# Performance work log

Hardware: AMD Instinct MI355X
Metric: run time of the kernel (lower is better)

## Reference

```python
import jax, jax.numpy as jnp
import numpy as np

S, B, D, E = 257, 64, 768, 8
H = 4 * D  # expert hidden dim

def quick_gelu(x):
    return x * jax.nn.sigmoid(1.702 * x)

def setup_inputs() -> dict:
    key = jax.random.key(0)
    ks = jax.random.split(key, 7)
    scale = 1.0 / np.sqrt(D)
    return {
        "x": jax.random.normal(ks[0], (S, B, D), dtype=jnp.float32),
        "W1": jax.random.normal(ks[1], (E, H, D), dtype=jnp.float32) * scale,   # fc1 weight per expert (out,in)
        "b1": jax.random.normal(ks[2], (E, H), dtype=jnp.float32) * 0.01,
        "W2": jax.random.normal(ks[3], (E, D, H), dtype=jnp.float32) * (1.0 / np.sqrt(H)),
        "b2": jax.random.normal(ks[4], (E, D), dtype=jnp.float32) * 0.01,
        "Wr": jax.random.normal(ks[5], (E, D), dtype=jnp.float32) * scale,       # router weight (E, d)
        "br": jnp.zeros((E,), dtype=jnp.float32),
    }

def reference(x, W1, b1, W2, b2, Wr, br):
    s, b, d = x.shape
    xf = x.reshape(s * b, d)                                  # [T, d]
    logits = xf @ Wr.T + br                                   # [T, E]
    probs = jax.nn.softmax(logits, axis=-1)                   # [T, E]
    # all-experts MLP, batched over the expert axis
    h = jnp.einsum('td,ehd->teh', xf, W1) + b1                # [T, E, 4d]
    h = quick_gelu(h)
    outs = jnp.einsum('teh,edh->ted', h, W2) + b2             # [T, E, d]
    y = jnp.einsum('ted,te->td', outs, probs)                 # router-weighted combine
    return y.reshape(s, b, d)
```

## Files before the change

kernel.cpp:

```cpp
#include <hip/hip_runtime.h>

typedef unsigned short u16;
typedef float f32x4 __attribute__((ext_vector_type(4)));
typedef short s16x8 __attribute__((ext_vector_type(8)));

#define T_TOK   16448L
#define D_DIM   768L
#define H_DIM   3072L
#define E_NUM   8L
#define M_PAD   16640L

__device__ __forceinline__ u16 f2bf(float f){
  unsigned u = __float_as_uint(f);
  u = u + 0x7FFFu + ((u >> 16) & 1u);
  return (u16)(u >> 16);
}
__device__ __forceinline__ unsigned f2bf2(float a, float b){
  return (unsigned)f2bf(a) | ((unsigned)f2bf(b) << 16);
}

__device__ __forceinline__ void gload_lds16(const u16* g, u16* s){
  __builtin_amdgcn_global_load_lds((const __attribute__((address_space(1))) void*)g,
                                   (__attribute__((address_space(3))) void*)s,
                                   16, 0, 0);
}

__device__ __forceinline__ int xcd_chunk(int idx, int n){
  const int q = n >> 3, r = n & 7, x = idx & 7;
  return (x < r ? x*(q+1) : r*(q+1) + (x-r)*q) + (idx >> 3);
}

__global__ void k_conv(const float* __restrict__ in, u16* __restrict__ outp,
                       long nValid, long nTotal){
  long i = (long)blockIdx.x * blockDim.x + threadIdx.x;
  long stride = (long)gridDim.x * blockDim.x;
  long n8 = nTotal >> 3;
  for (long v = i; v < n8; v += stride){
    long base = v << 3;
    uint4 o;
    if (base < nValid){
      const float4 f0 = *(const float4*)(in + base);
      const float4 f1 = *(const float4*)(in + base + 4);
      o.x = f2bf2(f0.x, f0.y); o.y = f2bf2(f0.z, f0.w);
      o.z = f2bf2(f1.x, f1.y); o.w = f2bf2(f1.z, f1.w);
    } else {
      o.x = 0u; o.y = 0u; o.z = 0u; o.w = 0u;
    }
    *(uint4*)(outp + base) = o;
  }
}

__global__ void k_router(const float* __restrict__ x, const float* __restrict__ Wr,
                         const float* __restrict__ br, float* __restrict__ probs){
  int w = (int)((blockIdx.x * (long)blockDim.x + threadIdx.x) >> 6);
  int lane = threadIdx.x & 63;
  if (w >= (int)T_TOK) return;
  const float* xr = x + (long)w * D_DIM;
  float l[8];
#pragma unroll
  for (int e = 0; e < 8; ++e) l[e] = 0.f;
#pragma unroll
  for (int c = 0; c < 3; ++c){
    const float4 xv = *(const float4*)(xr + c*256 + lane*4);
#pragma unroll
    for (int e = 0; e < 8; ++e){
      const float4 wv = *(const float4*)(Wr + (long)e*D_DIM + c*256 + lane*4);
      l[e] += xv.x*wv.x + xv.y*wv.y + xv.z*wv.z + xv.w*wv.w;
    }
  }
#pragma unroll
  for (int e = 0; e < 8; ++e){
#pragma unroll
    for (int off = 32; off > 0; off >>= 1) l[e] += __shfl_xor(l[e], off);
    l[e] += br[e];
  }
  float m = l[0];
#pragma unroll
  for (int e = 1; e < 8; ++e) m = fmaxf(m, l[e]);
  float s = 0.f;
#pragma unroll
  for (int e = 0; e < 8; ++e){ l[e] = __expf(l[e] - m); s += l[e]; }
  float inv = 1.f / s;
  if (lane == 0){
    float4 p0 = { l[0]*inv, l[1]*inv, l[2]*inv, l[3]*inv };
    float4 p1 = { l[4]*inv, l[5]*inv, l[6]*inv, l[7]*inv };
    *(float4*)(probs + (long)w*8)     = p0;
    *(float4*)(probs + (long)w*8 + 4) = p1;
  }
}

__device__ __forceinline__ void stage256(const u16* __restrict__ gbase, long ldk,
                                         u16* sbase, int l, int w){
  const int rw = l >> 3;
  const int c8 = (l & 7) ^ rw;
  const u16* g = gbase + (long)(w*8 + rw) * ldk + c8*8;
  u16* s = sbase + w*512;
#pragma unroll
  for (int i = 0; i < 4; ++i)
    gload_lds16(g + (long)(i*64) * ldk, s + i*4096);
}

__device__ __forceinline__ s16x8 ld_frag(const u16* S, int rbase, int c, int ln){
  const int r = rbase + ln;
  return *(const s16x8*)(S + (r << 6) + ((c ^ (r & 7)) << 3));
}

#define FENCE()  __builtin_amdgcn_sched_barrier(0)
#define BAR()    do{ FENCE(); __builtin_amdgcn_s_barrier(); FENCE(); }while(0)

__device__ __forceinline__ void gemm256(const u16* __restrict__ Ag, long lda,
                                        const u16* __restrict__ Bg, long ldb,
                                        int NT, u16* lds0, u16* lds1,
                                        int tid, f32x4 (&acc)[8][4]){
  const int l  = tid & 63, w = tid >> 6;
  const int wr = w >> 2,  wc = w & 3;
  const int g4 = l >> 4,  ln = l & 15;
  u16* cur = lds0; u16* nxt = lds1;

  stage256(Ag,       lda, cur,         l, w);
  stage256(Bg,       ldb, cur + 16384, l, w);
  stage256(Ag + 64,  lda, nxt,         l, w);
  stage256(Bg + 64,  ldb, nxt + 16384, l, w);
  FENCE();
  asm volatile("s_waitcnt vmcnt(8)" ::: "memory");
  BAR();

  for (int kt = 0; kt < NT; ++kt){
    const u16* As = cur;
    const u16* Bs = cur + 16384;
    s16x8 a0[8], b0[4], a1[8], b1[4];

#pragma unroll
    for (int ni = 0; ni < 4; ++ni) b0[ni] = ld_frag(Bs, wc*64 + ni*16, g4, ln);
#pragma unroll
    for (int mi = 0; mi < 8; ++mi) a0[mi] = ld_frag(As, wr*128 + mi*16, g4, ln);
#pragma unroll
    for (int mi = 0; mi < 8; ++mi)
#pragma unroll
      for (int ni = 0; ni < 4; ++ni)
        acc[mi][ni] = __builtin_amdgcn_mfma_f32_16x16x32_bf16(a0[mi], b0[ni], acc[mi][ni], 0, 0, 0);
#pragma unroll
    for (int ni = 0; ni < 4; ++ni) b1[ni] = ld_frag(Bs, wc*64 + ni*16, 4 + g4, ln);
#pragma unroll
    for (int mi = 0; mi < 8; ++mi) a1[mi] = ld_frag(As, wr*128 + mi*16, 4 + g4, ln);
#pragma unroll
    for (int mi = 0; mi < 8; ++mi)
#pragma unroll
      for (int ni = 0; ni < 4; ++ni)
        acc[mi][ni] = __builtin_amdgcn_mfma_f32_16x16x32_bf16(a1[mi], b1[ni], acc[mi][ni], 0, 0, 0);

    BAR();
    if (kt + 2 < NT){
      stage256(Ag + (long)(kt+2)*64, lda, cur,         l, w);
      stage256(Bg + (long)(kt+2)*64, ldb, cur + 16384, l, w);
      FENCE();
      asm volatile("s_waitcnt vmcnt(8)" ::: "memory");
    } else {
      FENCE();
      asm volatile("s_waitcnt vmcnt(0)" ::: "memory");
    }
    BAR();
    u16* t = cur; cur = nxt; nxt = t;
  }
}

__global__ __launch_bounds__(512, 2) void k_pair(const u16* __restrict__ xb,
                                                 const u16* __restrict__ w1b,
                                                 const float* __restrict__ b1,
                                                 const u16* __restrict__ w2b,
                                                 const float* __restrict__ b2,
                                                 const float* __restrict__ probs,
                                                 float* __restrict__ out,
                                                 const u16* __restrict__ hbR,
                                                 u16* __restrict__ hbW,
                                                 int e2, int t02,
                                                 int e1, int t01, int mt1, int n2){
  __shared__ alignas(16) u16 lds[2][32768];
  const int tid = threadIdx.x;
  const int l  = tid & 63, w = tid >> 6;
  const int wr = w >> 2,  wc = w & 3;
  const int g4 = l >> 4,  ln = l & 15;
  const int bx = (int)blockIdx.x;
  f32x4 acc[8][4] = {};

  if (bx < n2){
    const int wg = xcd_chunk(bx, n2);
    const int tx = wg / 3, ty = wg % 3;
    const int m0 = tx << 8, n0 = ty << 8;
    gemm256(hbR + (long)m0 * H_DIM, H_DIM,
            w2b + ((long)e2 * D_DIM + n0) * H_DIM, H_DIM,
            48, &lds[0][0], &lds[1][0], tid, acc);
    float bias[4];
#pragma unroll
    for (int ni = 0; ni < 4; ++ni) bias[ni] = b2[(long)e2*D_DIM + n0 + wc*64 + ni*16 + ln];
#pragma unroll
    for (int mi = 0; mi < 8; ++mi){
#pragma unroll
      for (int j = 0; j < 4; ++j){
        const int gt = t02 + m0 + wr*128 + mi*16 + g4*4 + j;
        if (gt < (int)T_TOK){
          const float p = probs[(long)gt*8 + e2];
          float* dst = out + (long)gt * D_DIM + n0 + wc*64;
#pragma unroll
          for (int ni = 0; ni < 4; ++ni){
            const float v = p * (acc[mi][ni][j] + bias[ni]);
            if (e2 == 0) dst[ni*16 + ln] = v;
            else         dst[ni*16 + ln] += v;
          }
        }
      }
    }
  } else {
    const int n1 = (int)gridDim.x - n2;
    const int wg = xcd_chunk(bx - n2, n1);
    const int tx = wg % mt1, ty = wg / mt1;
    const int m0 = tx << 8, n0 = ty << 8;
    gemm256(xb + (long)(t01 + m0) * D_DIM, D_DIM,
            w1b + ((long)e1 * H_DIM + n0) * D_DIM, D_DIM,
            12, &lds[0][0], &lds[1][0], tid, acc);
    float bias[4];
#pragma unroll
    for (int ni = 0; ni < 4; ++ni) bias[ni] = b1[(long)e1*H_DIM + n0 + wc*64 + ni*16 + ln];
#pragma unroll
    for (int mi = 0; mi < 8; ++mi){
#pragma unroll
      for (int j = 0; j < 4; ++j){
        const int r = m0 + wr*128 + mi*16 + g4*4 + j;
        u16* dst = hbW + (long)r * H_DIM + n0 + wc*64;
#pragma unroll
        for (int ni = 0; ni < 4; ++ni){
          const float v  = acc[mi][ni][j] + bias[ni];
          const float gl = v / (1.0f + __expf(-1.702f * v));
          dst[ni*16 + ln] = f2bf(gl);
        }
      }
    }
  }
}

extern "C" void kernel_launch(void* const* d_in, const int* in_sizes, int n_in,
                              void* d_out, int out_size, void* d_ws, size_t ws_size,
                              hipStream_t stream){
  const float* x  = (const float*)d_in[0];
  const float* W1 = (const float*)d_in[1];
  const float* b1 = (const float*)d_in[2];
  const float* W2 = (const float*)d_in[3];
  const float* b2 = (const float*)d_in[4];
  const float* Wr = (const float*)d_in[5];
  const float* br = (const float*)d_in[6];
  float* out = (float*)d_out;

  char* ws = (char*)d_ws;
  size_t off = 0;
  auto carve = [&](size_t bytes)->void*{
    void* p = ws + off; off += (bytes + 255) & ~(size_t)255; return p;
  };
  u16*   xb    = (u16*)  carve((size_t)M_PAD * D_DIM * 2);
  u16*   w1b   = (u16*)  carve((size_t)E_NUM * H_DIM * D_DIM * 2);
  u16*   w2b   = (u16*)  carve((size_t)E_NUM * D_DIM * H_DIM * 2);
  float* probs = (float*)carve((size_t)T_TOK * E_NUM * 4);
  u16*   hbA   = (u16*)  carve((size_t)8192 * H_DIM * 2);
  u16*   hbB   = (u16*)  carve((size_t)8448 * H_DIM * 2);

  k_conv<<<dim3(2048), dim3(256), 0, stream>>>(x,  xb,  T_TOK*D_DIM, M_PAD*D_DIM);
  k_conv<<<dim3(2048), dim3(256), 0, stream>>>(W1, w1b, E_NUM*H_DIM*D_DIM, E_NUM*H_DIM*D_DIM);
  k_conv<<<dim3(2048), dim3(256), 0, stream>>>(W2, w2b, E_NUM*D_DIM*H_DIM, E_NUM*D_DIM*H_DIM);
  k_router<<<dim3(4112), dim3(256), 0, stream>>>(x, Wr, br, probs);

  const int MTA = 32, MTB = 33;
  const int T0A = 0,  T0B = 8192;

  auto pair = [&](int e2, const u16* hbR, int t02, int mt2,
                  int e1, u16* hbW, int t01, int mt1){
    const int n2 = mt2 * 3, n1 = mt1 * 12;
    k_pair<<<dim3((unsigned)(n2 + n1)), dim3(512), 0, stream>>>(
        xb, w1b, b1, w2b, b2, probs, out, hbR, hbW,
        e2, t02, e1, t01, mt1, n2);
  };

  pair(0, nullptr, 0, 0, 0, hbA, T0A, MTA);
  for (int e = 0; e < 8; ++e){
    pair(e, hbA, T0A, MTA, e, hbB, T0B, MTB);
    if (e < 7) pair(e, hbB, T0B, MTB, e + 1, hbA, T0A, MTA);
  }
  pair(7, hbB, T0B, MTB, 0, nullptr, 0, 0);
}
```

Before: 2.104 ms.

## Switch GEMM mainloop to K=32 tiles with a four-stage LDS ring

Replaces the double-buffered K=64 staging in the shared 256x256 GEMM with K=32 slices held in a four-deep LDS ring buffer, using a new XOR swizzle and precomputed fragment offsets. Loads are issued three stages ahead with vmcnt waits that taper off near the tail. The goal is to hide more global-load latency behind the MFMAs. The cost is twice as many loop iterations and barriers, and less MFMA work per barrier.

```diff
diff --git a/kernel.cpp b/kernel.cpp
--- a/kernel.cpp
+++ b/kernel.cpp
@@ -89,78 +89,79 @@
   }
 }
 
-__device__ __forceinline__ void stage256(const u16* __restrict__ gbase, long ldk,
-                                         u16* sbase, int l, int w){
-  const int rw = l >> 3;
-  const int c8 = (l & 7) ^ rw;
-  const u16* g = gbase + (long)(w*8 + rw) * ldk + c8*8;
-  u16* s = sbase + w*512;
-#pragma unroll
-  for (int i = 0; i < 4; ++i)
-    gload_lds16(g + (long)(i*64) * ldk, s + i*4096);
-}
-
-__device__ __forceinline__ s16x8 ld_frag(const u16* S, int rbase, int c, int ln){
-  const int r = rbase + ln;
-  return *(const s16x8*)(S + (r << 6) + ((c ^ (r & 7)) << 3));
-}
-
 #define FENCE()  __builtin_amdgcn_sched_barrier(0)
 #define BAR()    do{ FENCE(); __builtin_amdgcn_s_barrier(); FENCE(); }while(0)
 
-__device__ __forceinline__ void gemm256(const u16* __restrict__ Ag, long lda,
-                                        const u16* __restrict__ Bg, long ldb,
-                                        int NT, u16* lds0, u16* lds1,
-                                        int tid, f32x4 (&acc)[8][4]){
+__device__ __forceinline__ void gemm256_k32(const u16* __restrict__ Ag, long lda,
+                                            const u16* __restrict__ Bg, long ldb,
+                                            int NT, u16* lds, int tid,
+                                            f32x4 (&acc)[8][4]){
   const int l  = tid & 63, w = tid >> 6;
   const int wr = w >> 2,  wc = w & 3;
   const int g4 = l >> 4,  ln = l & 15;
-  u16* cur = lds0; u16* nxt = lds1;
-
-  stage256(Ag,       lda, cur,         l, w);
-  stage256(Bg,       ldb, cur + 16384, l, w);
-  stage256(Ag + 64,  lda, nxt,         l, w);
-  stage256(Bg + 64,  ldb, nxt + 16384, l, w);
+
+  const int rw16 = l >> 2;
+  const int scol = ((l & 3) ^ (rw16 & 3)) << 3;
+  const u16* gA0 = Ag + (long)(      w*16 + rw16) * lda + scol;
+  const u16* gA1 = Ag + (long)(128 + w*16 + rw16) * lda + scol;
+  const u16* gB0 = Bg + (long)(      w*16 + rw16) * ldb + scol;
+  const u16* gB1 = Bg + (long)(128 + w*16 + rw16) * ldb + scol;
+  u16* dA0 = lds +        w*512;
+  u16* dA1 = lds + 4096 + w*512;
+  u16* dB0 = lds + 8192 +        w*512;
+  u16* dB1 = lds + 8192 + 4096 + w*512;
+
+  const int sw = (g4 ^ (ln & 3)) << 3;
+  int offA[8], offB[4];
+#pragma unroll
+  for (int mi = 0; mi < 8; ++mi) offA[mi] = (wr*128 + mi*16 + ln)*32 + sw;
+#pragma unroll
+  for (int ni = 0; ni < 4; ++ni) offB[ni] = 8192 + (wc*64 + ni*16 + ln)*32 + sw;
+
+#pragma unroll
+  for (int t = 0; t < 4; ++t){
+    const long ko = (long)t * 32;
+    const int  bo = t * 16384;
+    gload_lds16(gA0 + ko, dA0 + bo);
+    gload_lds16(gA1 + ko, dA1 + bo);
+    gload_lds16(gB0 + ko, dB0 + bo);
+    gload_lds16(gB1 + ko, dB1 + bo);
+  }
   FENCE();
-  asm volatile("s_waitcnt vmcnt(8)" ::: "memory");
+  asm volatile("s_waitcnt vmcnt(12)" ::: "memory");
   BAR();
 
   for (int kt = 0; kt < NT; ++kt){
-    const u16* As = cur;
-    const u16* Bs = cur + 16384;
-    s16x8 a0[8], b0[4], a1[8], b1[4];
-
-#pragma unroll
-    for (int ni = 0; ni < 4; ++ni) b0[ni] = ld_frag(Bs, wc*64 + ni*16, g4, ln);
-#pragma unroll
-    for (int mi = 0; mi < 8; ++mi) a0[mi] = ld_frag(As, wr*128 + mi*16, g4, ln);
+    const u16* base = lds + (kt & 3) * 16384;
+    s16x8 a[8], b[4];
+#pragma unroll
+    for (int ni = 0; ni < 4; ++ni) b[ni] = *(const s16x8*)(base + offB[ni]);
+#pragma unroll
+    for (int mi = 0; mi < 8; ++mi) a[mi] = *(const s16x8*)(base + offA[mi]);
 #pragma unroll
     for (int mi = 0; mi < 8; ++mi)
 #pragma unroll
       for (int ni = 0; ni < 4; ++ni)
-        acc[mi][ni] = __builtin_amdgcn_mfma_f32_16x16x32_bf16(a0[mi], b0[ni], acc[mi][ni], 0, 0, 0);
-#pragma unroll
-    for (int ni = 0; ni < 4; ++ni) b1[ni] = ld_frag(Bs, wc*64 + ni*16, 4 + g4, ln);
-#pragma unroll
-    for (int mi = 0; mi < 8; ++mi) a1[mi] = ld_frag(As, wr*128 + mi*16, 4 + g4, ln);
-#pragma unroll
-    for (int mi = 0; mi < 8; ++mi)
-#pragma unroll
-      for (int ni = 0; ni < 4; ++ni)
-        acc[mi][ni] = __builtin_amdgcn_mfma_f32_16x16x32_bf16(a1[mi], b1[ni], acc[mi][ni], 0, 0, 0);
-
-    BAR();
-    if (kt + 2 < NT){
-      stage256(Ag + (long)(kt+2)*64, lda, cur,         l, w);
-      stage256(Bg + (long)(kt+2)*64, ldb, cur + 16384, l, w);
+        acc[mi][ni] = __builtin_amdgcn_mfma_f32_16x16x32_bf16(a[mi], b[ni], acc[mi][ni], 0, 0, 0);
+
+    if (kt + 1 < NT){
+      BAR();
+      if (kt + 4 < NT){
+        const long ko = (long)(kt + 4) * 32;
+        const int  bo = (kt & 3) * 16384;
+        gload_lds16(gA0 + ko, dA0 + bo);
+        gload_lds16(gA1 + ko, dA1 + bo);
+        gload_lds16(gB0 + ko, dB0 + bo);
+        gload_lds16(gB1 + ko, dB1 + bo);
+      }
       FENCE();
-      asm volatile("s_waitcnt vmcnt(8)" ::: "memory");
-    } else {
-      FENCE();
-      asm volatile("s_waitcnt vmcnt(0)" ::: "memory");
-    }
-    BAR();
-    u16* t = cur; cur = nxt; nxt = t;
+      const int rem = NT - kt - 2;
+      if      (rem >= 3) asm volatile("s_waitcnt vmcnt(12)" ::: "memory");
+      else if (rem == 2) asm volatile("s_waitcnt vmcnt(8)"  ::: "memory");
+      else if (rem == 1) asm volatile("s_waitcnt vmcnt(4)"  ::: "memory");
+      else               asm volatile("s_waitcnt vmcnt(0)"  ::: "memory");
+      BAR();
+    }
   }
 }
 
@@ -175,7 +176,7 @@
                                                  u16* __restrict__ hbW,
                                                  int e2, int t02,
                                                  int e1, int t01, int mt1, int n2){
-  __shared__ alignas(16) u16 lds[2][32768];
+  __shared__ alignas(16) u16 lds[65536];
   const int tid = threadIdx.x;
   const int l  = tid & 63, w = tid >> 6;
   const int wr = w >> 2,  wc = w & 3;
@@ -187,9 +188,9 @@
     const int wg = xcd_chunk(bx, n2);
     const int tx = wg / 3, ty = wg % 3;
     const int m0 = tx << 8, n0 = ty << 8;
-    gemm256(hbR + (long)m0 * H_DIM, H_DIM,
-            w2b + ((long)e2 * D_DIM + n0) * H_DIM, H_DIM,
-            48, &lds[0][0], &lds[1][0], tid, acc);
+    gemm256_k32(hbR + (long)m0 * H_DIM, H_DIM,
+                w2b + ((long)e2 * D_DIM + n0) * H_DIM, H_DIM,
+                96, lds, tid, acc);
     float bias[4];
 #pragma unroll
     for (int ni = 0; ni < 4; ++ni) bias[ni] = b2[(long)e2*D_DIM + n0 + wc*64 + ni*16 + ln];
@@ -215,9 +216,9 @@
     const int wg = xcd_chunk(bx - n2, n1);
     const int tx = wg % mt1, ty = wg / mt1;
     const int m0 = tx << 8, n0 = ty << 8;
-    gemm256(xb + (long)(t01 + m0) * D_DIM, D_DIM,
-            w1b + ((long)e1 * H_DIM + n0) * D_DIM, D_DIM,
-            12, &lds[0][0], &lds[1][0], tid, acc);
+    gemm256_k32(xb + (long)(t01 + m0) * D_DIM, D_DIM,
+                w1b + ((long)e1 * H_DIM + n0) * D_DIM, D_DIM,
+                24, lds, tid, acc);
     float bias[4];
 #pragma unroll
     for (int ni = 0; ni < 4; ++ni) bias[ni] = b1[(long)e1*H_DIM + n0 + wc*64 + ni*16 + ln];
```

Result: slower. 2.218 ms (+5.4%).

## Interleave global-to-LDS staging with four MFMA sub-phases per K tile

Applied to the files above, without the earlier changes.

Restructures the 256x256 GEMM main loop into four quarter phases, each loading a subset of A/B fragments, issuing a slice of the next tiles' global-to-LDS copies, then running 16 MFMAs under raised wave priority. The goal is to spread memory traffic across the compute and cut register pressure, since only 4 A fragments are live at a time instead of 8. In exchange it adds more barriers per K step and a more intricate vmcnt accounting, which could stall waves or race on LDS reuse if the counts are off.

```diff
diff --git a/kernel.cpp b/kernel.cpp
--- a/kernel.cpp
+++ b/kernel.cpp
@@ -89,79 +89,111 @@
   }
 }
 
-__device__ __forceinline__ void stage256(const u16* __restrict__ gbase, long ldk,
-                                         u16* sbase, int l, int w){
-  const int rw = l >> 3;
-  const int c8 = (l & 7) ^ rw;
-  const u16* g = gbase + (long)(w*8 + rw) * ldk + c8*8;
-  u16* s = sbase + w*512;
-#pragma unroll
-  for (int i = 0; i < 4; ++i)
-    gload_lds16(g + (long)(i*64) * ldk, s + i*4096);
-}
+#define FENCE()  __builtin_amdgcn_sched_barrier(0)
+#define BAR()    do{ FENCE(); __builtin_amdgcn_s_barrier(); FENCE(); }while(0)
+#define LGK0()   do{ asm volatile("s_waitcnt lgkmcnt(0)" ::: "memory"); FENCE(); }while(0)
 
 __device__ __forceinline__ s16x8 ld_frag(const u16* S, int rbase, int c, int ln){
   const int r = rbase + ln;
   return *(const s16x8*)(S + (r << 6) + ((c ^ (r & 7)) << 3));
 }
 
-#define FENCE()  __builtin_amdgcn_sched_barrier(0)
-#define BAR()    do{ FENCE(); __builtin_amdgcn_s_barrier(); FENCE(); }while(0)
-
 __device__ __forceinline__ void gemm256(const u16* __restrict__ Ag, long lda,
                                         const u16* __restrict__ Bg, long ldb,
-                                        int NT, u16* lds0, u16* lds1,
-                                        int tid, f32x4 (&acc)[8][4]){
+                                        int NT, u16* lds, int tid,
+                                        f32x4 (&acc)[8][4]){
   const int l  = tid & 63, w = tid >> 6;
   const int wr = w >> 2,  wc = w & 3;
   const int g4 = l >> 4,  ln = l & 15;
-  u16* cur = lds0; u16* nxt = lds1;
-
-  stage256(Ag,       lda, cur,         l, w);
-  stage256(Bg,       ldb, cur + 16384, l, w);
-  stage256(Ag + 64,  lda, nxt,         l, w);
-  stage256(Bg + 64,  ldb, nxt + 16384, l, w);
+
+  const int rw = l >> 3;
+  const int c8 = (l & 7) ^ rw;
+  const u16* gA = Ag + (long)(w*8 + rw) * lda + c8*8;
+  const u16* gB = Bg + (long)(w*8 + rw) * ldb + c8*8;
+  u16* s0 = lds + w*512;
+#define SA(par,T,rnd) gload_lds16(gA + (long)(T)*64 + (long)(rnd)*64*lda, s0 + (par)*32768 + (rnd)*4096)
+#define SB(par,T,rnd) gload_lds16(gB + (long)(T)*64 + (long)(rnd)*64*ldb, s0 + (par)*32768 + 16384 + (rnd)*4096)
+
+#pragma unroll
+  for (int i = 0; i < 4; ++i) SA(0,0,i);
+#pragma unroll
+  for (int i = 0; i < 4; ++i) SB(0,0,i);
+  SA(1,1,0); SB(1,1,0); SA(1,1,2); SB(1,1,1);
   FENCE();
-  asm volatile("s_waitcnt vmcnt(8)" ::: "memory");
+  asm volatile("s_waitcnt vmcnt(4)" ::: "memory");
   BAR();
 
   for (int kt = 0; kt < NT; ++kt){
-    const u16* As = cur;
-    const u16* Bs = cur + 16384;
-    s16x8 a0[8], b0[4], a1[8], b1[4];
+    const int par = kt & 1, oth = par ^ 1;
+    const u16* As = lds + par * 32768;
+    const u16* Bs = As + 16384;
+    const bool st1 = (kt + 1 < NT), st2 = (kt + 2 < NT);
+    s16x8 aL[4], aH[4], b0[4], b1[4];
 
 #pragma unroll
     for (int ni = 0; ni < 4; ++ni) b0[ni] = ld_frag(Bs, wc*64 + ni*16, g4, ln);
 #pragma unroll
-    for (int mi = 0; mi < 8; ++mi) a0[mi] = ld_frag(As, wr*128 + mi*16, g4, ln);
-#pragma unroll
-    for (int mi = 0; mi < 8; ++mi)
+    for (int mi = 0; mi < 4; ++mi) aL[mi] = ld_frag(As, wr*128 + mi*16, g4, ln);
+    if (st1){ SA(oth, kt+1, 1); SB(oth, kt+1, 2); }
+    BAR(); LGK0();
+    __builtin_amdgcn_s_setprio(1);
+#pragma unroll
+    for (int mi = 0; mi < 4; ++mi)
 #pragma unroll
       for (int ni = 0; ni < 4; ++ni)
-        acc[mi][ni] = __builtin_amdgcn_mfma_f32_16x16x32_bf16(a0[mi], b0[ni], acc[mi][ni], 0, 0, 0);
+        acc[mi][ni] = __builtin_amdgcn_mfma_f32_16x16x32_bf16(aL[mi], b0[ni], acc[mi][ni], 0, 0, 0);
+    __builtin_amdgcn_s_setprio(0);
+    BAR();
+
 #pragma unroll
     for (int ni = 0; ni < 4; ++ni) b1[ni] = ld_frag(Bs, wc*64 + ni*16, 4 + g4, ln);
 #pragma unroll
-    for (int mi = 0; mi < 8; ++mi) a1[mi] = ld_frag(As, wr*128 + mi*16, 4 + g4, ln);
-#pragma unroll
-    for (int mi = 0; mi < 8; ++mi)
+    for (int mi = 0; mi < 4; ++mi) aL[mi] = ld_frag(As, wr*128 + mi*16, 4 + g4, ln);
+    if (st1){ SA(oth, kt+1, 3); SB(oth, kt+1, 3); }
+    BAR(); LGK0();
+    __builtin_amdgcn_s_setprio(1);
+#pragma unroll
+    for (int mi = 0; mi < 4; ++mi)
 #pragma unroll
       for (int ni = 0; ni < 4; ++ni)
-        acc[mi][ni] = __builtin_amdgcn_mfma_f32_16x16x32_bf16(a1[mi], b1[ni], acc[mi][ni], 0, 0, 0);
-
+        acc[mi][ni] = __builtin_amdgcn_mfma_f32_16x16x32_bf16(aL[mi], b1[ni], acc[mi][ni], 0, 0, 0);
+    __builtin_amdgcn_s_setprio(0);
     BAR();
-    if (kt + 2 < NT){
-      stage256(Ag + (long)(kt+2)*64, lda, cur,         l, w);
-      stage256(Bg + (long)(kt+2)*64, ldb, cur + 16384, l, w);
+
+#pragma unroll
+    for (int mi = 0; mi < 4; ++mi) aH[mi] = ld_frag(As, wr*128 + 64 + mi*16, g4, ln);
+    if (st2){ SA(par, kt+2, 0); SB(par, kt+2, 0); }
+    BAR(); LGK0();
+    __builtin_amdgcn_s_setprio(1);
+#pragma unroll
+    for (int mi = 0; mi < 4; ++mi)
+#pragma unroll
+      for (int ni = 0; ni < 4; ++ni)
+        acc[mi+4][ni] = __builtin_amdgcn_mfma_f32_16x16x32_bf16(aH[mi], b0[ni], acc[mi+4][ni], 0, 0, 0);
+    __builtin_amdgcn_s_setprio(0);
+    BAR();
+
+#pragma unroll
+    for (int mi = 0; mi < 4; ++mi) aH[mi] = ld_frag(As, wr*128 + 64 + mi*16, 4 + g4, ln);
+    if (st2){ SA(par, kt+2, 2); SB(par, kt+2, 1); }
+    BAR(); LGK0();
+    __builtin_amdgcn_s_setprio(1);
+#pragma unroll
+    for (int mi = 0; mi < 4; ++mi)
+#pragma unroll
+      for (int ni = 0; ni < 4; ++ni)
+        acc[mi+4][ni] = __builtin_amdgcn_mfma_f32_16x16x32_bf16(aH[mi], b1[ni], acc[mi+4][ni], 0, 0, 0);
+    __builtin_amdgcn_s_setprio(0);
+
+    if (st1){
       FENCE();
-      asm volatile("s_waitcnt vmcnt(8)" ::: "memory");
-    } else {
-      FENCE();
-      asm volatile("s_waitcnt vmcnt(0)" ::: "memory");
-    }
-    BAR();
-    u16* t = cur; cur = nxt; nxt = t;
-  }
+      if (st2) asm volatile("s_waitcnt vmcnt(4)" ::: "memory");
+      else     asm volatile("s_waitcnt vmcnt(0)" ::: "memory");
+      BAR();
+    }
+  }
+#undef SA
+#undef SB
 }
 
 __global__ __launch_bounds__(512, 2) void k_pair(const u16* __restrict__ xb,
@@ -175,7 +207,7 @@
                                                  u16* __restrict__ hbW,
                                                  int e2, int t02,
                                                  int e1, int t01, int mt1, int n2){
-  __shared__ alignas(16) u16 lds[2][32768];
+  __shared__ alignas(16) u16 lds[65536];
   const int tid = threadIdx.x;
   const int l  = tid & 63, w = tid >> 6;
   const int wr = w >> 2,  wc = w & 3;
@@ -189,7 +221,7 @@
     const int m0 = tx << 8, n0 = ty << 8;
     gemm256(hbR + (long)m0 * H_DIM, H_DIM,
             w2b + ((long)e2 * D_DIM + n0) * H_DIM, H_DIM,
-            48, &lds[0][0], &lds[1][0], tid, acc);
+            48, lds, tid, acc);
     float bias[4];
 #pragma unroll
     for (int ni = 0; ni < 4; ++ni) bias[ni] = b2[(long)e2*D_DIM + n0 + wc*64 + ni*16 + ln];
@@ -217,7 +249,7 @@
     const int m0 = tx << 8, n0 = ty << 8;
     gemm256(xb + (long)(t01 + m0) * D_DIM, D_DIM,
             w1b + ((long)e1 * H_DIM + n0) * D_DIM, D_DIM,
-            12, &lds[0][0], &lds[1][0], tid, acc);
+            12, lds, tid, acc);
     float bias[4];
 #pragma unroll
     for (int ni = 0; ni < 4; ++ni) bias[ni] = b1[(long)e1*H_DIM + n0 + wc*64 + ni*16 + ln];
```

Result: faster. 2.003 ms (-4.8%).

## Shrink GEMM tiles to 128x128 with single-buffered LDS and 256-thread blocks

Applied to the files above, without the earlier changes.

Replaces the 256x256 double-buffered GEMM tile (512 threads, 128KB LDS, prefetch two stages ahead) with a 128x128 single-buffered tile using 4 waves and 32KB LDS, with precomputed swizzled fragment offsets. Grid sizes, token padding and hidden buffer sizes are adjusted to match the smaller tiles. This raises block count and occupancy and cuts per-block LDS and register use. In exchange it loses global-to-LDS prefetch overlap, since loads are now waited on with a barrier every k-step, and it lowers operand reuse per tile.

```diff
diff --git a/kernel.cpp b/kernel.cpp
--- a/kernel.cpp
+++ b/kernel.cpp
@@ -8,7 +8,7 @@
 #define D_DIM   768L
 #define H_DIM   3072L
 #define E_NUM   8L
-#define M_PAD   16640L
+#define M_PAD   16512L
 
 __device__ __forceinline__ u16 f2bf(float f){
   unsigned u = __float_as_uint(f);
@@ -89,115 +89,102 @@
   }
 }
 
-__device__ __forceinline__ void stage256(const u16* __restrict__ gbase, long ldk,
-                                         u16* sbase, int l, int w){
+__device__ __forceinline__ void gemm128(const u16* __restrict__ Ag, long lda,
+                                        const u16* __restrict__ Bg, long ldb,
+                                        int NT, u16* As, u16* Bs,
+                                        int tid, f32x4 (&acc)[4][4]){
+  const int l  = tid & 63, w = tid >> 6;
+  const int wr = w >> 1,  wc = w & 1;
+  const int g4 = l >> 4,  ln = l & 15;
+
   const int rw = l >> 3;
   const int c8 = (l & 7) ^ rw;
-  const u16* g = gbase + (long)(w*8 + rw) * ldk + c8*8;
-  u16* s = sbase + w*512;
-#pragma unroll
-  for (int i = 0; i < 4; ++i)
-    gload_lds16(g + (long)(i*64) * ldk, s + i*4096);
-}
-
-__device__ __forceinline__ s16x8 ld_frag(const u16* S, int rbase, int c, int ln){
-  const int r = rbase + ln;
-  return *(const s16x8*)(S + (r << 6) + ((c ^ (r & 7)) << 3));
-}
-
-#define FENCE()  __builtin_amdgcn_sched_barrier(0)
-#define BAR()    do{ FENCE(); __builtin_amdgcn_s_barrier(); FENCE(); }while(0)
-
-__device__ __forceinline__ void gemm256(const u16* __restrict__ Ag, long lda,
-                                        const u16* __restrict__ Bg, long ldb,
-                                        int NT, u16* lds0, u16* lds1,
-                                        int tid, f32x4 (&acc)[8][4]){
-  const int l  = tid & 63, w = tid >> 6;
-  const int wr = w >> 2,  wc = w & 3;
-  const int g4 = l >> 4,  ln = l & 15;
-  u16* cur = lds0; u16* nxt = lds1;
-
-  stage256(Ag,       lda, cur,         l, w);
-  stage256(Bg,       ldb, cur + 16384, l, w);
-  stage256(Ag + 64,  lda, nxt,         l, w);
-  stage256(Bg + 64,  ldb, nxt + 16384, l, w);
-  FENCE();
-  asm volatile("s_waitcnt vmcnt(8)" ::: "memory");
-  BAR();
+  const u16* pA = Ag + (long)(w*8 + rw) * lda + c8*8;
+  const u16* pB = Bg + (long)(w*8 + rw) * ldb + c8*8;
+  const long sA = 32 * lda, sB = 32 * ldb;
+  u16* dA = As + w*512;
+  u16* dB = Bs + w*512;
+
+  int offA[2][4], offB[2][4];
+#pragma unroll
+  for (int kk = 0; kk < 2; ++kk)
+#pragma unroll
+    for (int i = 0; i < 4; ++i){
+      const int co = (((kk<<2) | g4) ^ (ln & 7)) << 3;
+      offA[kk][i] = (wr*64 + i*16 + ln)*64 + co;
+      offB[kk][i] = (wc*64 + i*16 + ln)*64 + co;
+    }
 
   for (int kt = 0; kt < NT; ++kt){
-    const u16* As = cur;
-    const u16* Bs = cur + 16384;
-    s16x8 a0[8], b0[4], a1[8], b1[4];
-
-#pragma unroll
-    for (int ni = 0; ni < 4; ++ni) b0[ni] = ld_frag(Bs, wc*64 + ni*16, g4, ln);
-#pragma unroll
-    for (int mi = 0; mi < 8; ++mi) a0[mi] = ld_frag(As, wr*128 + mi*16, g4, ln);
-#pragma unroll
-    for (int mi = 0; mi < 8; ++mi)
+    gload_lds16(pA,        dA);
+    gload_lds16(pA +   sA, dA + 2048);
+    gload_lds16(pA + 2*sA, dA + 4096);
+    gload_lds16(pA + 3*sA, dA + 6144);
+    gload_lds16(pB,        dB);
+    gload_lds16(pB +   sB, dB + 2048);
+    gload_lds16(pB + 2*sB, dB + 4096);
+    gload_lds16(pB + 3*sB, dB + 6144);
+    pA += 64; pB += 64;
+    __syncthreads();
+
+    s16x8 a0[4], b0[4], a1[4], b1[4];
+#pragma unroll
+    for (int i = 0; i < 4; ++i) a0[i] = *(const s16x8*)(As + offA[0][i]);
+#pragma unroll
+    for (int i = 0; i < 4; ++i) b0[i] = *(const s16x8*)(Bs + offB[0][i]);
+#pragma unroll
+    for (int mi = 0; mi < 4; ++mi)
 #pragma unroll
       for (int ni = 0; ni < 4; ++ni)
         acc[mi][ni] = __builtin_amdgcn_mfma_f32_16x16x32_bf16(a0[mi], b0[ni], acc[mi][ni], 0, 0, 0);
 #pragma unroll
-    for (int ni = 0; ni < 4; ++ni) b1[ni] = ld_frag(Bs, wc*64 + ni*16, 4 + g4, ln);
-#pragma unroll
-    for (int mi = 0; mi < 8; ++mi) a1[mi] = ld_frag(As, wr*128 + mi*16, 4 + g4, ln);
-#pragma unroll
-    for (int mi = 0; mi < 8; ++mi)
+    for (int i = 0; i < 4; ++i) a1[i] = *(const s16x8*)(As + offA[1][i]);
+#pragma unroll
+    for (int i = 0; i < 4; ++i) b1[i] = *(const s16x8*)(Bs + offB[1][i]);
+#pragma unroll
+    for (int mi = 0; mi < 4; ++mi)
 #pragma unroll
       for (int ni = 0; ni < 4; ++ni)
         acc[mi][ni] = __builtin_amdgcn_mfma_f32_16x16x32_bf16(a1[mi], b1[ni], acc[mi][ni], 0, 0, 0);
-
-    BAR();
-    if (kt + 2 < NT){
-      stage256(Ag + (long)(kt+2)*64, lda, cur,         l, w);
-      stage256(Bg + (long)(kt+2)*64, ldb, cur + 16384, l, w);
-      FENCE();
-      asm volatile("s_waitcnt vmcnt(8)" ::: "memory");
-    } else {
-      FENCE();
-      asm volatile("s_waitcnt vmcnt(0)" ::: "memory");
-    }
-    BAR();
-    u16* t = cur; cur = nxt; nxt = t;
-  }
-}
-
-__global__ __launch_bounds__(512, 2) void k_pair(const u16* __restrict__ xb,
-                                                 const u16* __restrict__ w1b,
-                                                 const float* __restrict__ b1,
-                                                 const u16* __restrict__ w2b,
-                                                 const float* __restrict__ b2,
-                                                 const float* __restrict__ probs,
-                                                 float* __restrict__ out,
-                                                 const u16* __restrict__ hbR,
-                                                 u16* __restrict__ hbW,
-                                                 int e2, int t02,
-                                                 int e1, int t01, int mt1, int n2){
-  __shared__ alignas(16) u16 lds[2][32768];
+    __syncthreads();
+  }
+}
+
+__global__ __launch_bounds__(256) void k_pair(const u16* __restrict__ xb,
+                                              const u16* __restrict__ w1b,
+                                              const float* __restrict__ b1,
+                                              const u16* __restrict__ w2b,
+                                              const float* __restrict__ b2,
+                                              const float* __restrict__ probs,
+                                              float* __restrict__ out,
+                                              const u16* __restrict__ hbR,
+                                              u16* __restrict__ hbW,
+                                              int e2, int t02,
+                                              int e1, int t01, int mt1, int n2){
+  __shared__ alignas(16) u16 As[8192];
+  __shared__ alignas(16) u16 Bs[8192];
   const int tid = threadIdx.x;
   const int l  = tid & 63, w = tid >> 6;
-  const int wr = w >> 2,  wc = w & 3;
+  const int wr = w >> 1,  wc = w & 1;
   const int g4 = l >> 4,  ln = l & 15;
   const int bx = (int)blockIdx.x;
-  f32x4 acc[8][4] = {};
+  f32x4 acc[4][4] = {};
 
   if (bx < n2){
     const int wg = xcd_chunk(bx, n2);
-    const int tx = wg / 3, ty = wg % 3;
-    const int m0 = tx << 8, n0 = ty << 8;
-    gemm256(hbR + (long)m0 * H_DIM, H_DIM,
+    const int tx = wg / 6, ty = wg % 6;
+    const int m0 = tx << 7, n0 = ty << 7;
+    gemm128(hbR + (long)m0 * H_DIM, H_DIM,
             w2b + ((long)e2 * D_DIM + n0) * H_DIM, H_DIM,
-            48, &lds[0][0], &lds[1][0], tid, acc);
+            48, As, Bs, tid, acc);
     float bias[4];
 #pragma unroll
     for (int ni = 0; ni < 4; ++ni) bias[ni] = b2[(long)e2*D_DIM + n0 + wc*64 + ni*16 + ln];
 #pragma unroll
-    for (int mi = 0; mi < 8; ++mi){
+    for (int mi = 0; mi < 4; ++mi){
 #pragma unroll
       for (int j = 0; j < 4; ++j){
-        const int gt = t02 + m0 + wr*128 + mi*16 + g4*4 + j;
+        const int gt = t02 + m0 + wr*64 + mi*16 + g4*4 + j;
         if (gt < (int)T_TOK){
           const float p = probs[(long)gt*8 + e2];
           float* dst = out + (long)gt * D_DIM + n0 + wc*64;
@@ -214,18 +201,18 @@
     const int n1 = (int)gridDim.x - n2;
     const int wg = xcd_chunk(bx - n2, n1);
     const int tx = wg % mt1, ty = wg / mt1;
-    const int m0 = tx << 8, n0 = ty << 8;
-    gemm256(xb + (long)(t01 + m0) * D_DIM, D_DIM,
+    const int m0 = tx << 7, n0 = ty << 7;
+    gemm128(xb + (long)(t01 + m0) * D_DIM, D_DIM,
             w1b + ((long)e1 * H_DIM + n0) * D_DIM, D_DIM,
-            12, &lds[0][0], &lds[1][0], tid, acc);
+            12, As, Bs, tid, acc);
     float bias[4];
 #pragma unroll
     for (int ni = 0; ni < 4; ++ni) bias[ni] = b1[(long)e1*H_DIM + n0 + wc*64 + ni*16 + ln];
 #pragma unroll
-    for (int mi = 0; mi < 8; ++mi){
+    for (int mi = 0; mi < 4; ++mi){
 #pragma unroll
       for (int j = 0; j < 4; ++j){
-        const int r = m0 + wr*128 + mi*16 + g4*4 + j;
+        const int r = m0 + wr*64 + mi*16 + g4*4 + j;
         u16* dst = hbW + (long)r * H_DIM + n0 + wc*64;
 #pragma unroll
         for (int ni = 0; ni < 4; ++ni){
@@ -260,20 +247,20 @@
   u16*   w2b   = (u16*)  carve((size_t)E_NUM * D_DIM * H_DIM * 2);
   float* probs = (float*)carve((size_t)T_TOK * E_NUM * 4);
   u16*   hbA   = (u16*)  carve((size_t)8192 * H_DIM * 2);
-  u16*   hbB   = (u16*)  carve((size_t)8448 * H_DIM * 2);
+  u16*   hbB   = (u16*)  carve((size_t)8320 * H_DIM * 2);
 
   k_conv<<<dim3(2048), dim3(256), 0, stream>>>(x,  xb,  T_TOK*D_DIM, M_PAD*D_DIM);
   k_conv<<<dim3(2048), dim3(256), 0, stream>>>(W1, w1b, E_NUM*H_DIM*D_DIM, E_NUM*H_DIM*D_DIM);
   k_conv<<<dim3(2048), dim3(256), 0, stream>>>(W2, w2b, E_NUM*D_DIM*H_DIM, E_NUM*D_DIM*H_DIM);
   k_router<<<dim3(4112), dim3(256), 0, stream>>>(x, Wr, br, probs);
 
-  const int MTA = 32, MTB = 33;
+  const int MTA = 64, MTB = 65;
   const int T0A = 0,  T0B = 8192;
 
   auto pair = [&](int e2, const u16* hbR, int t02, int mt2,
                   int e1, u16* hbW, int t01, int mt1){
-    const int n2 = mt2 * 3, n1 = mt1 * 12;
-    k_pair<<<dim3((unsigned)(n2 + n1)), dim3(512), 0, stream>>>(
+    const int n2 = mt2 * 6, n1 = mt1 * 24;
+    k_pair<<<dim3((unsigned)(n2 + n1)), dim3(256), 0, stream>>>(
         xb, w1b, b1, w2b, b2, probs, out, hbR, hbW,
         e2, t02, e1, t01, mt1, n2);
   };
```

Result: no change. 2.110 ms (+0.3%).
